# Optimization experiments

Hardware: AMD Instinct MI355X
Metric: run time of the kernel (lower is better)

## Reference

```python
import jax, jax.numpy as jnp
import numpy as np

LOGIT_TEMP = 0.1
EPS = 1e-8


def _compute_logits(px, tgt, emb):
    # px: [F, D] selected projected frames; tgt: [F] int labels; emb: [C, D]
    pxn = px / jnp.maximum(jnp.linalg.norm(px, axis=-1, keepdims=True), EPS)
    embn = emb / jnp.maximum(jnp.linalg.norm(emb, axis=-1, keepdims=True), EPS)
    pos = jnp.sum(pxn * embn[tgt], axis=-1)          # [F] cosine to positive
    neg = jnp.einsum('fd,cd->fc', pxn, embn)          # [F, C] cosine to all classes
    # neg_is_pos: emb row of target exactly equals the neg row (torch: (pos==negs).all(-1))
    row_eq = jnp.all(emb[:, None, :] == emb[None, :, :], axis=-1)  # [C, C]
    neg_is_pos = row_eq[:, tgt].T                     # [F, C]
    neg = jnp.where(neg_is_pos, -jnp.inf, neg / LOGIT_TEMP)
    return jnp.concatenate([pos[:, None] / LOGIT_TEMP, neg], axis=1)  # [F, C+1]


def setup_inputs() -> dict:
    key = jax.random.key(0)
    k = jax.random.split(key, 7)
    B, T, De, Df, C = 16, 1500, 768, 256, 500
    n_m = n_u = 12000
    x = jax.random.normal(k[0], (B, T, De), dtype=jnp.float32)
    label = jax.random.randint(k[1], (B, T), 0, C, dtype=jnp.int32)
    mask_m = jax.random.randint(k[2], (n_m,), 0, B * T, dtype=jnp.int32)
    mask_u = jax.random.randint(k[3], (n_u,), 0, B * T, dtype=jnp.int32)
    W = jax.random.normal(k[4], (De, Df), dtype=jnp.float32) * 0.02
    b = jnp.zeros((Df,), dtype=jnp.float32)
    emb = jax.random.uniform(k[5], (C, Df), dtype=jnp.float32)  # torch uniform_ init
    return {"x": x, "label": label, "mask_m": mask_m, "mask_u": mask_u,
            "W": W, "b": b, "emb": emb}


def reference(x, label, mask_m, mask_u, W, b, emb):
    proj = jnp.einsum('bte,ef->btf', x, W) + b        # final_proj
    Df = proj.shape[-1]
    pf = proj.reshape(-1, Df)                          # [B*T, Df]
    lf = label.reshape(-1)
    logit_m = _compute_logits(pf[mask_m], lf[mask_m], emb)
    logit_u = _compute_logits(pf[mask_u], lf[mask_u], emb)
    return (logit_m, logit_u)
```

## Files before the change

kernel.cpp:

```cpp
#include <hip/hip_runtime.h>
#include <math.h>

typedef unsigned short u16;
typedef unsigned int   u32;
typedef __attribute__((ext_vector_type(4))) float          f32x4;
typedef __attribute__((ext_vector_type(8))) short          short8;
typedef __attribute__((ext_vector_type(4))) unsigned short u16x4;
typedef __attribute__((ext_vector_type(8))) unsigned short u16x8;

#define NSEL   24000
#define NHALF  12000
#define D_E    768
#define D_F    256
#define NC     500
#define NCP    512
#define MASK_VAL -3.0e38f

__device__ inline u16 f2bf(float f) {
    u32 u = __float_as_uint(f);
    return (u16)((u + 0x7FFFu + ((u >> 16) & 1u)) >> 16);
}

__global__ void prep_w(const float* __restrict__ W, u16* __restrict__ Wt) {
    __shared__ float tile[32][33];
    const int k0 = blockIdx.x * 32, n0 = blockIdx.y * 32;
    const int tx = threadIdx.x, ty = threadIdx.y;
    #pragma unroll
    for (int i = 0; i < 4; ++i)
        tile[ty + i * 8][tx] = W[(size_t)(k0 + ty + i * 8) * D_F + n0 + tx];
    __syncthreads();
    #pragma unroll
    for (int i = 0; i < 4; ++i)
        Wt[(size_t)(n0 + ty + i * 8) * D_E + k0 + tx] = f2bf(tile[tx][ty + i * 8]);
}

__global__ void prep_emb(const float* __restrict__ emb, u16* __restrict__ Et) {
    const int c = blockIdx.x, t = threadIdx.x;
    if (c >= NC) { Et[(size_t)c * D_F + t] = 0; return; }
    const float v = emb[(size_t)c * D_F + t];
    float sq = v * v;
    #pragma unroll
    for (int o = 32; o > 0; o >>= 1) sq += __shfl_xor(sq, o);
    __shared__ float ws2[4];
    if ((t & 63) == 0) ws2[t >> 6] = sq;
    __syncthreads();
    const float tot = ws2[0] + ws2[1] + ws2[2] + ws2[3];
    const float inv = 1.0f / fmaxf(sqrtf(tot), 1e-8f);
    Et[(size_t)c * D_F + t] = f2bf(v * inv);
}

__global__ void eqcls_kernel(const float* __restrict__ emb, u16* __restrict__ eqcls) {
    const int c = blockIdx.x;
    if (c >= NC) { if (threadIdx.x == 0) eqcls[c] = 0xFFFFu; return; }
    const int t = threadIdx.x;
    int best = c;
    const float4* ra = (const float4*)(emb + (size_t)c * D_F);
    for (int d = t; d < c; d += 256) {
        const float4* rb = (const float4*)(emb + (size_t)d * D_F);
        bool eq = true;
        for (int k = 0; k < D_F / 4; ++k) {
            const float4 a = ra[k], bq = rb[k];
            if (a.x != bq.x || a.y != bq.y || a.z != bq.z || a.w != bq.w) { eq = false; break; }
        }
        if (eq) best = min(best, d);
    }
    #pragma unroll
    for (int o = 32; o > 0; o >>= 1) best = min(best, __shfl_xor(best, o));
    __shared__ int red[4];
    if ((t & 63) == 0) red[t >> 6] = best;
    __syncthreads();
    if (t == 0) eqcls[c] = (u16)min(min(red[0], red[1]), min(red[2], red[3]));
}

__global__ void proj_mfma(const float* __restrict__ x, const u16* __restrict__ Wt,
                          const float* __restrict__ b, float* __restrict__ pxn) {
    __shared__ u16  As[64 * 32];
    __shared__ u16  Bs[256 * 32];
    __shared__ float bs[256];
    __shared__ float sq[64];
    const int tid  = threadIdx.x;
    const int lane = tid & 63, wid = tid >> 6;
    const int row0 = blockIdx.x * 64;
    bs[tid] = b[tid];

    f32x4 acc[4][4] = {};
    const int ar  = tid >> 3, ac4 = tid & 7;
    const int bn  = tid >> 2, slot = tid & 3;

    for (int kt = 0; kt < D_E / 32; ++kt) {
        const int k0 = kt * 32;
        #pragma unroll
        for (int rr = 0; rr < 2; ++rr) {
            const int r = ar + rr * 32;
            const float4 xv = *(const float4*)(x + (size_t)(row0 + r) * D_E + k0 + ac4 * 4);
            u16x4 h; h.x = f2bf(xv.x); h.y = f2bf(xv.y); h.z = f2bf(xv.z); h.w = f2bf(xv.w);
            *(u16x4*)(As + r * 32 + ((ac4 * 4) ^ ((r & 3) << 3))) = h;
        }
        #pragma unroll
        for (int p = 0; p < 4; ++p) {
            const int n = bn + p * 64;
            const u16x8 w = *(const u16x8*)(Wt + (size_t)n * D_E + k0 + slot * 8);
            *(u16x8*)(Bs + n * 32 + ((slot * 8) ^ ((n & 3) << 3))) = w;
        }
        __syncthreads();
        const int lg = lane >> 4, l15 = lane & 15, swz = (lane & 3) << 3;
        short8 a[4], bf[4];
        #pragma unroll
        for (int m = 0; m < 4; ++m) {
            const int r = m * 16 + l15;
            a[m] = *(const short8*)(As + r * 32 + ((lg * 8) ^ swz));
        }
        #pragma unroll
        for (int n = 0; n < 4; ++n) {
            const int c = wid * 64 + n * 16 + l15;
            bf[n] = *(const short8*)(Bs + c * 32 + ((lg * 8) ^ swz));
        }
        #pragma unroll
        for (int m = 0; m < 4; ++m)
            #pragma unroll
            for (int n = 0; n < 4; ++n)
                acc[m][n] = __builtin_amdgcn_mfma_f32_16x16x32_bf16(a[m], bf[n], acc[m][n], 0, 0, 0);
        __syncthreads();
    }

    if (tid < 64) sq[tid] = 0.0f;
    __syncthreads();
    const int lg = lane >> 4, l15 = lane & 15;
    #pragma unroll
    for (int m = 0; m < 4; ++m)
        #pragma unroll
        for (int n = 0; n < 4; ++n) {
            const float bb = bs[wid * 64 + n * 16 + l15];
            #pragma unroll
            for (int q = 0; q < 4; ++q) acc[m][n][q] += bb;
        }
    #pragma unroll
    for (int m = 0; m < 4; ++m)
        #pragma unroll
        for (int q = 0; q < 4; ++q) {
            float p = 0.0f;
            #pragma unroll
            for (int n = 0; n < 4; ++n) p += acc[m][n][q] * acc[m][n][q];
            p += __shfl_xor(p, 1); p += __shfl_xor(p, 2);
            p += __shfl_xor(p, 4); p += __shfl_xor(p, 8);
            if (l15 == 0) atomicAdd(&sq[m * 16 + lg * 4 + q], p);
        }
    __syncthreads();
    #pragma unroll
    for (int m = 0; m < 4; ++m)
        #pragma unroll
        for (int q = 0; q < 4; ++q) {
            const int row = m * 16 + lg * 4 + q;
            const float inv = 1.0f / fmaxf(sqrtf(sq[row]), 1e-8f);
            #pragma unroll
            for (int n = 0; n < 4; ++n) {
                const int col = wid * 64 + n * 16 + l15;
                pxn[(size_t)(row0 + row) * D_F + col] = acc[m][n][q] * inv;
            }
        }
}

__global__ void logits_mfma(const float* __restrict__ pxn, const u16* __restrict__ Et,
                            const u16* __restrict__ eqcls_g, const int* __restrict__ label,
                            const int* __restrict__ mm, const int* __restrict__ mu,
                            float* __restrict__ out) {
    __shared__ u16 As[64 * 32];
    __shared__ u16 Bs[256 * 32];
    __shared__ int sel_s[64];
    __shared__ int tgt_s[64];
    __shared__ u16 tcls_s[64];
    __shared__ u16 ecls_s[256];
    const int tid  = threadIdx.x;
    const int lane = tid & 63, wid = tid >> 6;
    const int row0 = blockIdx.x * 64;
    const int nb   = blockIdx.y * 256;

    if (tid < 64) {
        const int i   = row0 + tid;
        const int sel = (i < NHALF) ? mm[i] : mu[i - NHALF];
        sel_s[tid] = sel;
        const int tg = label[sel];
        tgt_s[tid]  = tg;
        tcls_s[tid] = eqcls_g[tg];
    }
    ecls_s[tid] = eqcls_g[nb + tid];
    __syncthreads();

    f32x4 acc[4][4] = {};
    const int ar = tid >> 3, ac4 = tid & 7;
    const int bn = tid >> 2, slot = tid & 3;

    for (int kt = 0; kt < D_F / 32; ++kt) {
        const int k0 = kt * 32;
        #pragma unroll
        for (int rr = 0; rr < 2; ++rr) {
            const int r = ar + rr * 32;
            const float4 xv = *(const float4*)(pxn + (size_t)sel_s[r] * D_F + k0 + ac4 * 4);
            u16x4 h; h.x = f2bf(xv.x); h.y = f2bf(xv.y); h.z = f2bf(xv.z); h.w = f2bf(xv.w);
            *(u16x4*)(As + r * 32 + ((ac4 * 4) ^ ((r & 3) << 3))) = h;
        }
        #pragma unroll
        for (int p = 0; p < 4; ++p) {
            const int n = bn + p * 64;
            const u16x8 w = *(const u16x8*)(Et + (size_t)(nb + n) * D_F + k0 + slot * 8);
            *(u16x8*)(Bs + n * 32 + ((slot * 8) ^ ((n & 3) << 3))) = w;
        }
        __syncthreads();
        const int lg = lane >> 4, l15 = lane & 15, swz = (lane & 3) << 3;
        short8 a[4], bf[4];
        #pragma unroll
        for (int m = 0; m < 4; ++m) {
            const int r = m * 16 + l15;
            a[m] = *(const short8*)(As + r * 32 + ((lg * 8) ^ swz));
        }
        #pragma unroll
        for (int n = 0; n < 4; ++n) {
            const int c = wid * 64 + n * 16 + l15;
            bf[n] = *(const short8*)(Bs + c * 32 + ((lg * 8) ^ swz));
        }
        #pragma unroll
        for (int m = 0; m < 4; ++m)
            #pragma unroll
            for (int n = 0; n < 4; ++n)
                acc[m][n] = __builtin_amdgcn_mfma_f32_16x16x32_bf16(a[m], bf[n], acc[m][n], 0, 0, 0);
        __syncthreads();
    }

    const int lg = lane >> 4, l15 = lane & 15;
    #pragma unroll
    for (int m = 0; m < 4; ++m)
        #pragma unroll
        for (int q = 0; q < 4; ++q) {
            const int row = m * 16 + lg * 4 + q;
            const int i   = row0 + row;
            const u16 tc  = tcls_s[row];
            const int tg  = tgt_s[row];
            float* orow   = out + (size_t)i * (NC + 1);
            #pragma unroll
            for (int n = 0; n < 4; ++n) {
                const int col16 = wid * 64 + n * 16 + l15;
                const int c     = nb + col16;
                if (c < NC) {
                    const float val = acc[m][n][q] * 10.0f;
                    orow[1 + c] = (ecls_s[col16] == tc) ? MASK_VAL : val;
                    if (c == tg) orow[0] = val;
                }
            }
        }
}

extern "C" void kernel_launch(void* const* d_in, const int* in_sizes, int n_in,
                              void* d_out, int out_size, void* d_ws, size_t ws_size,
                              hipStream_t stream) {
    const float* x     = (const float*)d_in[0];
    const int*   label = (const int*)  d_in[1];
    const int*   mm    = (const int*)  d_in[2];
    const int*   mu    = (const int*)  d_in[3];
    const float* W     = (const float*)d_in[4];
    const float* b     = (const float*)d_in[5];
    const float* emb   = (const float*)d_in[6];
    float* out = (float*)d_out;

    float* pxn  = (float*)d_ws;
    u16*   Wt   = (u16*)(pxn + (size_t)NSEL * D_F);
    u16*   Et   = Wt + (size_t)D_F * D_E;
    u16*   eqc  = Et + (size_t)NCP * D_F;

    prep_w      <<<dim3(D_E / 32, D_F / 32), dim3(32, 8), 0, stream>>>(W, Wt);
    prep_emb    <<<NCP, 256, 0, stream>>>(emb, Et);
    eqcls_kernel<<<NCP, 256, 0, stream>>>(emb, eqc);
    proj_mfma   <<<NSEL / 64, 256, 0, stream>>>(x, Wt, b, pxn);
    logits_mfma <<<dim3(NSEL / 64, 2), 256, 0, stream>>>(pxn, Et, eqc, label, mm, mu, out);
}
```

Measured before the change: 191.0 us.

## Load MFMA fragments directly from global memory and store normalized projections as bf16

Both GEMM kernels drop their shared-memory staging and the barriers around it. Each lane now loads its MFMA operand fragments straight from global memory, with x converted to bf16 in registers, and the row tile shrinks to 32 rows to double the block count. The normalized projection buffer is written as bf16 instead of fp32, which halves the intermediate write and the gathered re-read in the logits kernel and removes the second conversion. Launch bounds are added for occupancy. In exchange, W and emb fragments are re-read from L2 by every block rather than shared through LDS.

Result: slower. 227.3 us (+19.0%).

```diff
diff --git a/kernel.cpp b/kernel.cpp
--- a/kernel.cpp
+++ b/kernel.cpp
@@ -5,7 +5,7 @@
 typedef unsigned int   u32;
 typedef __attribute__((ext_vector_type(4))) float          f32x4;
 typedef __attribute__((ext_vector_type(8))) short          short8;
-typedef __attribute__((ext_vector_type(4))) unsigned short u16x4;
+typedef __attribute__((ext_vector_type(4))) unsigned int   u32x4;
 typedef __attribute__((ext_vector_type(8))) unsigned short u16x8;
 
 #define NSEL   24000
@@ -19,6 +19,19 @@
 __device__ inline u16 f2bf(float f) {
     u32 u = __float_as_uint(f);
     return (u16)((u + 0x7FFFu + ((u >> 16) & 1u)) >> 16);
+}
+
+__device__ inline u32 pack2(float lo, float hi) {
+    return (u32)f2bf(lo) | ((u32)f2bf(hi) << 16);
+}
+
+__device__ inline short8 pack8(const float4 lo, const float4 hi) {
+    u32x4 w;
+    w.x = pack2(lo.x, lo.y);
+    w.y = pack2(lo.z, lo.w);
+    w.z = pack2(hi.x, hi.y);
+    w.w = pack2(hi.z, hi.w);
+    return __builtin_bit_cast(short8, w);
 }
 
 __global__ void prep_w(const float* __restrict__ W, u16* __restrict__ Wt) {
@@ -72,70 +85,62 @@
     if (t == 0) eqcls[c] = (u16)min(min(red[0], red[1]), min(red[2], red[3]));
 }
 
-__global__ void proj_mfma(const float* __restrict__ x, const u16* __restrict__ Wt,
-                          const float* __restrict__ b, float* __restrict__ pxn) {
-    __shared__ u16  As[64 * 32];
-    __shared__ u16  Bs[256 * 32];
-    __shared__ float bs[256];
-    __shared__ float sq[64];
+__global__ __launch_bounds__(256, 4)
+void proj_mfma(const float* __restrict__ x, const u16* __restrict__ Wt,
+               const float* __restrict__ b, u16* __restrict__ pxnb) {
     const int tid  = threadIdx.x;
     const int lane = tid & 63, wid = tid >> 6;
-    const int row0 = blockIdx.x * 64;
-    bs[tid] = b[tid];
-
-    f32x4 acc[4][4] = {};
-    const int ar  = tid >> 3, ac4 = tid & 7;
-    const int bn  = tid >> 2, slot = tid & 3;
-
+    const int lg   = lane >> 4, l15 = lane & 15;
+    const int row0 = blockIdx.x * 32;
+
+    const float* xa0 = x + (size_t)(row0 + l15)      * D_E + lg * 8;
+    const float* xa1 = x + (size_t)(row0 + 16 + l15) * D_E + lg * 8;
+    const u16* wb0 = Wt + (size_t)(wid * 64 +  0 + l15) * D_E + lg * 8;
+    const u16* wb1 = Wt + (size_t)(wid * 64 + 16 + l15) * D_E + lg * 8;
+    const u16* wb2 = Wt + (size_t)(wid * 64 + 32 + l15) * D_E + lg * 8;
+    const u16* wb3 = Wt + (size_t)(wid * 64 + 48 + l15) * D_E + lg * 8;
+
+    f32x4 acc[2][4] = {};
+
+    #pragma unroll 4
     for (int kt = 0; kt < D_E / 32; ++kt) {
         const int k0 = kt * 32;
-        #pragma unroll
-        for (int rr = 0; rr < 2; ++rr) {
-            const int r = ar + rr * 32;
-            const float4 xv = *(const float4*)(x + (size_t)(row0 + r) * D_E + k0 + ac4 * 4);
-            u16x4 h; h.x = f2bf(xv.x); h.y = f2bf(xv.y); h.z = f2bf(xv.z); h.w = f2bf(xv.w);
-            *(u16x4*)(As + r * 32 + ((ac4 * 4) ^ ((r & 3) << 3))) = h;
-        }
-        #pragma unroll
-        for (int p = 0; p < 4; ++p) {
-            const int n = bn + p * 64;
-            const u16x8 w = *(const u16x8*)(Wt + (size_t)n * D_E + k0 + slot * 8);
-            *(u16x8*)(Bs + n * 32 + ((slot * 8) ^ ((n & 3) << 3))) = w;
-        }
-        __syncthreads();
-        const int lg = lane >> 4, l15 = lane & 15, swz = (lane & 3) << 3;
-        short8 a[4], bf[4];
-        #pragma unroll
-        for (int m = 0; m < 4; ++m) {
-            const int r = m * 16 + l15;
-            a[m] = *(const short8*)(As + r * 32 + ((lg * 8) ^ swz));
-        }
-        #pragma unroll
-        for (int n = 0; n < 4; ++n) {
-            const int c = wid * 64 + n * 16 + l15;
-            bf[n] = *(const short8*)(Bs + c * 32 + ((lg * 8) ^ swz));
-        }
-        #pragma unroll
-        for (int m = 0; m < 4; ++m)
-            #pragma unroll
-            for (int n = 0; n < 4; ++n)
-                acc[m][n] = __builtin_amdgcn_mfma_f32_16x16x32_bf16(a[m], bf[n], acc[m][n], 0, 0, 0);
-        __syncthreads();
-    }
-
-    if (tid < 64) sq[tid] = 0.0f;
-    __syncthreads();
-    const int lg = lane >> 4, l15 = lane & 15;
-    #pragma unroll
-    for (int m = 0; m < 4; ++m)
-        #pragma unroll
-        for (int n = 0; n < 4; ++n) {
-            const float bb = bs[wid * 64 + n * 16 + l15];
-            #pragma unroll
-            for (int q = 0; q < 4; ++q) acc[m][n][q] += bb;
-        }
-    #pragma unroll
-    for (int m = 0; m < 4; ++m)
+        const float4 a0l = *(const float4*)(xa0 + k0);
+        const float4 a0h = *(const float4*)(xa0 + k0 + 4);
+        const float4 a1l = *(const float4*)(xa1 + k0);
+        const float4 a1h = *(const float4*)(xa1 + k0 + 4);
+        const short8 a0 = pack8(a0l, a0h);
+        const short8 a1 = pack8(a1l, a1h);
+        const short8 b0 = __builtin_bit_cast(short8, *(const u16x8*)(wb0 + k0));
+        const short8 b1 = __builtin_bit_cast(short8, *(const u16x8*)(wb1 + k0));
+        const short8 b2 = __builtin_bit_cast(short8, *(const u16x8*)(wb2 + k0));
+        const short8 b3 = __builtin_bit_cast(short8, *(const u16x8*)(wb3 + k0));
+        acc[0][0] = __builtin_amdgcn_mfma_f32_16x16x32_bf16(a0, b0, acc[0][0], 0, 0, 0);
+        acc[0][1] = __builtin_amdgcn_mfma_f32_16x16x32_bf16(a0, b1, acc[0][1], 0, 0, 0);
+        acc[0][2] = __builtin_amdgcn_mfma_f32_16x16x32_bf16(a0, b2, acc[0][2], 0, 0, 0);
+        acc[0][3] = __builtin_amdgcn_mfma_f32_16x16x32_bf16(a0, b3, acc[0][3], 0, 0, 0);
+        acc[1][0] = __builtin_amdgcn_mfma_f32_16x16x32_bf16(a1, b0, acc[1][0], 0, 0, 0);
+        acc[1][1] = __builtin_amdgcn_mfma_f32_16x16x32_bf16(a1, b1, acc[1][1], 0, 0, 0);
+        acc[1][2] = __builtin_amdgcn_mfma_f32_16x16x32_bf16(a1, b2, acc[1][2], 0, 0, 0);
+        acc[1][3] = __builtin_amdgcn_mfma_f32_16x16x32_bf16(a1, b3, acc[1][3], 0, 0, 0);
+    }
+
+    __shared__ float sq[32];
+    if (tid < 32) sq[tid] = 0.0f;
+    __syncthreads();
+
+    float bb[4];
+    #pragma unroll
+    for (int n = 0; n < 4; ++n) bb[n] = b[wid * 64 + n * 16 + l15];
+    #pragma unroll
+    for (int m = 0; m < 2; ++m)
+        #pragma unroll
+        for (int n = 0; n < 4; ++n)
+            #pragma unroll
+            for (int q = 0; q < 4; ++q) acc[m][n][q] += bb[n];
+
+    #pragma unroll
+    for (int m = 0; m < 2; ++m)
         #pragma unroll
         for (int q = 0; q < 4; ++q) {
             float p = 0.0f;
@@ -146,8 +151,9 @@
             if (l15 == 0) atomicAdd(&sq[m * 16 + lg * 4 + q], p);
         }
     __syncthreads();
-    #pragma unroll
-    for (int m = 0; m < 4; ++m)
+
+    #pragma unroll
+    for (int m = 0; m < 2; ++m)
         #pragma unroll
         for (int q = 0; q < 4; ++q) {
             const int row = m * 16 + lg * 4 + q;
@@ -155,27 +161,27 @@
             #pragma unroll
             for (int n = 0; n < 4; ++n) {
                 const int col = wid * 64 + n * 16 + l15;
-                pxn[(size_t)(row0 + row) * D_F + col] = acc[m][n][q] * inv;
+                pxnb[(size_t)(row0 + row) * D_F + col] = f2bf(acc[m][n][q] * inv);
             }
         }
 }
 
-__global__ void logits_mfma(const float* __restrict__ pxn, const u16* __restrict__ Et,
-                            const u16* __restrict__ eqcls_g, const int* __restrict__ label,
-                            const int* __restrict__ mm, const int* __restrict__ mu,
-                            float* __restrict__ out) {
-    __shared__ u16 As[64 * 32];
-    __shared__ u16 Bs[256 * 32];
-    __shared__ int sel_s[64];
-    __shared__ int tgt_s[64];
-    __shared__ u16 tcls_s[64];
+__global__ __launch_bounds__(256, 4)
+void logits_mfma(const u16* __restrict__ pxnb, const u16* __restrict__ Et,
+                 const u16* __restrict__ eqcls_g, const int* __restrict__ label,
+                 const int* __restrict__ mm, const int* __restrict__ mu,
+                 float* __restrict__ out) {
+    __shared__ int sel_s[32];
+    __shared__ int tgt_s[32];
+    __shared__ u16 tcls_s[32];
     __shared__ u16 ecls_s[256];
     const int tid  = threadIdx.x;
     const int lane = tid & 63, wid = tid >> 6;
-    const int row0 = blockIdx.x * 64;
+    const int lg   = lane >> 4, l15 = lane & 15;
+    const int row0 = blockIdx.x * 32;
     const int nb   = blockIdx.y * 256;
 
-    if (tid < 64) {
+    if (tid < 32) {
         const int i   = row0 + tid;
         const int sel = (i < NHALF) ? mm[i] : mu[i - NHALF];
         sel_s[tid] = sel;
@@ -186,56 +192,43 @@
     ecls_s[tid] = eqcls_g[nb + tid];
     __syncthreads();
 
-    f32x4 acc[4][4] = {};
-    const int ar = tid >> 3, ac4 = tid & 7;
-    const int bn = tid >> 2, slot = tid & 3;
-
+    const u16* pa0 = pxnb + (size_t)sel_s[l15]      * D_F + lg * 8;
+    const u16* pa1 = pxnb + (size_t)sel_s[16 + l15] * D_F + lg * 8;
+    const u16* eb0 = Et + (size_t)(nb + wid * 64 +  0 + l15) * D_F + lg * 8;
+    const u16* eb1 = Et + (size_t)(nb + wid * 64 + 16 + l15) * D_F + lg * 8;
+    const u16* eb2 = Et + (size_t)(nb + wid * 64 + 32 + l15) * D_F + lg * 8;
+    const u16* eb3 = Et + (size_t)(nb + wid * 64 + 48 + l15) * D_F + lg * 8;
+
+    f32x4 acc[2][4] = {};
+
+    #pragma unroll
     for (int kt = 0; kt < D_F / 32; ++kt) {
         const int k0 = kt * 32;
-        #pragma unroll
-        for (int rr = 0; rr < 2; ++rr) {
-            const int r = ar + rr * 32;
-            const float4 xv = *(const float4*)(pxn + (size_t)sel_s[r] * D_F + k0 + ac4 * 4);
-            u16x4 h; h.x = f2bf(xv.x); h.y = f2bf(xv.y); h.z = f2bf(xv.z); h.w = f2bf(xv.w);
-            *(u16x4*)(As + r * 32 + ((ac4 * 4) ^ ((r & 3) << 3))) = h;
-        }
-        #pragma unroll
-        for (int p = 0; p < 4; ++p) {
-            const int n = bn + p * 64;
-            const u16x8 w = *(const u16x8*)(Et + (size_t)(nb + n) * D_F + k0 + slot * 8);
-            *(u16x8*)(Bs + n * 32 + ((slot * 8) ^ ((n & 3) << 3))) = w;
-        }
-        __syncthreads();
-        const int lg = lane >> 4, l15 = lane & 15, swz = (lane & 3) << 3;
-        short8 a[4], bf[4];
-        #pragma unroll
-        for (int m = 0; m < 4; ++m) {
-            const int r = m * 16 + l15;
-            a[m] = *(const short8*)(As + r * 32 + ((lg * 8) ^ swz));
-        }
-        #pragma unroll
-        for (int n = 0; n < 4; ++n) {
-            const int c = wid * 64 + n * 16 + l15;
-            bf[n] = *(const short8*)(Bs + c * 32 + ((lg * 8) ^ swz));
-        }
-        #pragma unroll
-        for (int m = 0; m < 4; ++m)
-            #pragma unroll
-            for (int n = 0; n < 4; ++n)
-                acc[m][n] = __builtin_amdgcn_mfma_f32_16x16x32_bf16(a[m], bf[n], acc[m][n], 0, 0, 0);
-        __syncthreads();
-    }
-
-    const int lg = lane >> 4, l15 = lane & 15;
-    #pragma unroll
-    for (int m = 0; m < 4; ++m)
+        const short8 a0 = __builtin_bit_cast(short8, *(const u16x8*)(pa0 + k0));
+        const short8 a1 = __builtin_bit_cast(short8, *(const u16x8*)(pa1 + k0));
+        const short8 b0 = __builtin_bit_cast(short8, *(const u16x8*)(eb0 + k0));
+        const short8 b1 = __builtin_bit_cast(short8, *(const u16x8*)(eb1 + k0));
+        const short8 b2 = __builtin_bit_cast(short8, *(const u16x8*)(eb2 + k0));
+        const short8 b3 = __builtin_bit_cast(short8, *(const u16x8*)(eb3 + k0));
+        acc[0][0] = __builtin_amdgcn_mfma_f32_16x16x32_bf16(a0, b0, acc[0][0], 0, 0, 0);
+        acc[0][1] = __builtin_amdgcn_mfma_f32_16x16x32_bf16(a0, b1, acc[0][1], 0, 0, 0);
+        acc[0][2] = __builtin_amdgcn_mfma_f32_16x16x32_bf16(a0, b2, acc[0][2], 0, 0, 0);
+        acc[0][3] = __builtin_amdgcn_mfma_f32_16x16x32_bf16(a0, b3, acc[0][3], 0, 0, 0);
+        acc[1][0] = __builtin_amdgcn_mfma_f32_16x16x32_bf16(a1, b0, acc[1][0], 0, 0, 0);
+        acc[1][1] = __builtin_amdgcn_mfma_f32_16x16x32_bf16(a1, b1, acc[1][1], 0, 0, 0);
+        acc[1][2] = __builtin_amdgcn_mfma_f32_16x16x32_bf16(a1, b2, acc[1][2], 0, 0, 0);
+        acc[1][3] = __builtin_amdgcn_mfma_f32_16x16x32_bf16(a1, b3, acc[1][3], 0, 0, 0);
+    }
+
+    #pragma unroll
+    for (int m = 0; m < 2; ++m)
         #pragma unroll
         for (int q = 0; q < 4; ++q) {
-            const int row = m * 16 + lg * 4 + q;
-            const int i   = row0 + row;
-            const u16 tc  = tcls_s[row];
-            const int tg  = tgt_s[row];
-            float* orow   = out + (size_t)i * (NC + 1);
+            const int rloc = m * 16 + lg * 4 + q;
+            const int i    = row0 + rloc;
+            const u16 tc   = tcls_s[rloc];
+            const int tg   = tgt_s[rloc];
+            float* orow    = out + (size_t)i * (NC + 1);
             #pragma unroll
             for (int n = 0; n < 4; ++n) {
                 const int col16 = wid * 64 + n * 16 + l15;
@@ -261,14 +254,14 @@
     const float* emb   = (const float*)d_in[6];
     float* out = (float*)d_out;
 
-    float* pxn  = (float*)d_ws;
-    u16*   Wt   = (u16*)(pxn + (size_t)NSEL * D_F);
-    u16*   Et   = Wt + (size_t)D_F * D_E;
-    u16*   eqc  = Et + (size_t)NCP * D_F;
+    u16* pxnb = (u16*)d_ws;
+    u16* Wt   = pxnb + (size_t)NSEL * D_F;
+    u16* Et   = Wt + (size_t)D_F * D_E;
+    u16* eqc  = Et + (size_t)NCP * D_F;
 
     prep_w      <<<dim3(D_E / 32, D_F / 32), dim3(32, 8), 0, stream>>>(W, Wt);
     prep_emb    <<<NCP, 256, 0, stream>>>(emb, Et);
     eqcls_kernel<<<NCP, 256, 0, stream>>>(emb, eqc);
-    proj_mfma   <<<NSEL / 64, 256, 0, stream>>>(x, Wt, b, pxn);
-    logits_mfma <<<dim3(NSEL / 64, 2), 256, 0, stream>>>(pxn, Et, eqc, label, mm, mu, out);
-}
+    proj_mfma   <<<NSEL / 32, 256, 0, stream>>>(x, Wt, b, pxnb);
+    logits_mfma <<<dim3(NSEL / 32, 2), 256, 0, stream>>>(pxnb, Et, eqc, label, mm, mu, out);
+}
```
